# Kernel tuning notes

Hardware: AMD Instinct MI355X
Metric: run time of the kernel (lower is better)

The kernel has to match this reference:

```python
import jax, jax.numpy as jnp
import numpy as np

N = 50000          # nodes
E = 800000         # edges (before self loops)
H = 4              # attention heads
C = 64             # per-head channels
D_IN = 256
NEG_ATT = 0.2      # GATConv attention LeakyReLU slope
NEG_ACT = 0.01     # nn.LeakyReLU default slope
EPS = 1e-5
MLP_DIMS = [64, 32, 16, 2]


def _gat_layer(x, src, dst, W, a_src, a_dst, b, concat):
    """PyG GATConv: gather -> segment-softmax over dst -> scatter-add."""
    n = x.shape[0]
    h = (x @ W).reshape(n, H, C)                       # [N,H,C]
    s = (h * a_src).sum(-1)                            # [N,H]
    d = (h * a_dst).sum(-1)                            # [N,H]
    e = jax.nn.leaky_relu(s[src] + d[dst], NEG_ATT)    # [E',H]
    m = jax.ops.segment_max(e, dst, num_segments=n)    # per-dst max (self loops -> no empty segs)
    w = jnp.exp(e - m[dst])
    den = jax.ops.segment_sum(w, dst, num_segments=n)
    alpha = w / den[dst]                               # [E',H]
    out = jax.ops.segment_sum(alpha[:, :, None] * h[src], dst, num_segments=n)  # [N,H,C]
    out = out.reshape(n, H * C) if concat else out.mean(axis=1)
    return out + b


def _graph_norm(x, w, b, a):
    mu = x.mean(axis=0, keepdims=True)
    y = x - a * mu
    var = (y * y).mean(axis=0, keepdims=True)
    return w * y * jax.lax.rsqrt(var + EPS) + b


def setup_inputs() -> dict:
    key = jax.random.key(0)
    ks = jax.random.split(key, 40)
    d = {
        'x': jax.random.normal(ks[0], (N, D_IN), dtype=jnp.float32),
        'edge_index': jax.random.randint(ks[1], (2, E), 0, N, dtype=jnp.int64),
    }
    dims_in = [D_IN, H * C, H * C]
    norm_dims = [H * C, H * C, C]
    k = 2
    for i in range(3):
        fan = dims_in[i]
        d[f'W{i}'] = jax.random.normal(ks[k], (fan, H * C), dtype=jnp.float32) / np.sqrt(fan); k += 1
        d[f'as{i}'] = jax.random.normal(ks[k], (H, C), dtype=jnp.float32) / np.sqrt(C); k += 1
        d[f'ad{i}'] = jax.random.normal(ks[k], (H, C), dtype=jnp.float32) / np.sqrt(C); k += 1
        d[f'b{i}'] = jnp.zeros((norm_dims[i],), dtype=jnp.float32)
        d[f'gw{i}'] = jnp.ones((norm_dims[i],), dtype=jnp.float32)
        d[f'gb{i}'] = jnp.zeros((norm_dims[i],), dtype=jnp.float32)
        d[f'ga{i}'] = jnp.ones((norm_dims[i],), dtype=jnp.float32)
    for j in range(3):
        fi, fo = MLP_DIMS[j], MLP_DIMS[j + 1]
        d[f'mW{j}'] = jax.random.normal(ks[k], (fi, fo), dtype=jnp.float32) / np.sqrt(fi); k += 1
        d[f'mb{j}'] = jnp.zeros((fo,), dtype=jnp.float32)
    return d


def reference(x, edge_index,
              W0, as0, ad0, b0, gw0, gb0, ga0,
              W1, as1, ad1, b1, gw1, gb1, ga1,
              W2, as2, ad2, b2, gw2, gb2, ga2,
              mW0, mb0, mW1, mb1, mW2, mb2):
    n = x.shape[0]
    loop = jnp.arange(n, dtype=edge_index.dtype)
    src = jnp.concatenate([edge_index[0], loop])   # add self loops (PyG default)
    dst = jnp.concatenate([edge_index[1], loop])

    h = _gat_layer(x, src, dst, W0, as0, ad0, b0, concat=True)
    h = jax.nn.leaky_relu(_graph_norm(h, gw0, gb0, ga0), NEG_ACT)
    h = _gat_layer(h, src, dst, W1, as1, ad1, b1, concat=True)
    h = jax.nn.leaky_relu(_graph_norm(h, gw1, gb1, ga1), NEG_ACT)
    h = _gat_layer(h, src, dst, W2, as2, ad2, b2, concat=False)
    h = jax.nn.leaky_relu(_graph_norm(h, gw2, gb2, ga2), NEG_ACT)

    h = jax.nn.relu(h @ mW0 + mb0)
    h = jax.nn.relu(h @ mW1 + mb1)
    return h @ mW2 + mb2
```

## Files before the change

kernel.cpp:

```cpp
#include <hip/hip_runtime.h>

#define NN 50000
#define EE 800000
#define ET 850000
#define HH 4
#define CC 64
#define FDIM 256

#define SCAN_BLK 512
#define SCAN_NB ((NN + SCAN_BLK - 1) / SCAN_BLK)

typedef unsigned short ushort;
typedef __bf16 bf16x8 __attribute__((ext_vector_type(8)));
typedef float floatx4 __attribute__((ext_vector_type(4)));
typedef ushort ushort8v __attribute__((ext_vector_type(8)));
struct ushort4s { ushort x, y, z, w; };

__device__ __forceinline__ ushort f2bf(float f) {
  union { float f; unsigned u; } v; v.f = f;
  unsigned r = v.u + 0x7fffu + ((v.u >> 16) & 1u);
  return (ushort)(r >> 16);
}
__device__ __forceinline__ float bf2f(ushort u) {
  return __uint_as_float(((unsigned)u) << 16);
}

__device__ __forceinline__ void gload16(const void* gsrc, void* ldst) {
  __builtin_amdgcn_global_load_lds(
      (const __attribute__((address_space(1))) void*)gsrc,
      (__attribute__((address_space(3))) void*)ldst, 16, 0, 0);
}

__device__ __forceinline__ int get_edge(const void* p, int is64, long long idx) {
  if (is64) return (int)((const long long*)p)[idx];
  return ((const int*)p)[idx];
}

__global__ void degree_kernel(const void* eidx, int is64, int* deg) {
  int k = blockIdx.x * blockDim.x + threadIdx.x;
  if (k >= ET) return;
  int dst = (k < EE) ? get_edge(eidx, is64, (long long)EE + k) : (k - EE);
  atomicAdd(&deg[dst], 1);
}

__global__ __launch_bounds__(SCAN_BLK) void scan1_kernel(const int* __restrict__ deg,
                                                         int* __restrict__ rowptr,
                                                         int* __restrict__ bsum) {
  __shared__ int sm[SCAN_BLK];
  int t = threadIdx.x;
  int i = blockIdx.x * SCAN_BLK + t;
  int v = (i < NN) ? deg[i] : 0;
  sm[t] = v;
  __syncthreads();
#pragma unroll
  for (int o = 1; o < SCAN_BLK; o <<= 1) {
    int u = (t >= o) ? sm[t - o] : 0;
    __syncthreads();
    sm[t] += u;
    __syncthreads();
  }
  if (i < NN) rowptr[i] = sm[t] - v;
  if (t == SCAN_BLK - 1) bsum[blockIdx.x] = sm[t];
}

__global__ __launch_bounds__(128) void scan2_kernel(const int* __restrict__ bsum,
                                                    int* __restrict__ boff,
                                                    int* __restrict__ rowptr) {
  __shared__ int sm[128];
  int t = threadIdx.x;
  int v = (t < SCAN_NB) ? bsum[t] : 0;
  sm[t] = v;
  __syncthreads();
#pragma unroll
  for (int o = 1; o < 128; o <<= 1) {
    int u = (t >= o) ? sm[t - o] : 0;
    __syncthreads();
    sm[t] += u;
    __syncthreads();
  }
  if (t < SCAN_NB) boff[t] = sm[t] - v;
  if (t == 0) rowptr[NN] = ET;
}

__global__ __launch_bounds__(SCAN_BLK) void scan3_kernel(int* __restrict__ rowptr,
                                                         int* __restrict__ cursor,
                                                         const int* __restrict__ boff) {
  int i = blockIdx.x * SCAN_BLK + threadIdx.x;
  if (i >= NN) return;
  int v = rowptr[i] + boff[blockIdx.x];
  rowptr[i] = v;
  cursor[i] = v;
}

__global__ void fill_kernel(const void* eidx, int is64, int* cursor, int* csr_src) {
  int k = blockIdx.x * blockDim.x + threadIdx.x;
  if (k >= ET) return;
  int src, dst;
  if (k < EE) {
    src = get_edge(eidx, is64, k);
    dst = get_edge(eidx, is64, (long long)EE + k);
  } else {
    src = dst = k - EE;
  }
  int pos = atomicAdd(&cursor[dst], 1);
  csr_src[pos] = src;
}

__global__ void conv_w_kernel(const float* __restrict__ W0, const float* __restrict__ W1,
                              const float* __restrict__ W2,
                              ushort* __restrict__ T0, ushort* __restrict__ T1,
                              ushort* __restrict__ T2) {
  const float* W = (blockIdx.y == 0) ? W0 : (blockIdx.y == 1) ? W1 : W2;
  ushort* Wt = (blockIdx.y == 0) ? T0 : (blockIdx.y == 1) ? T1 : T2;
  int idx = blockIdx.x * 256 + threadIdx.x;
  int k = idx >> 8, n = idx & 255;
  Wt[n * 256 + k] = f2bf(W[idx]);
}

__global__ __launch_bounds__(256) void cvt_x_kernel(const float* __restrict__ x,
                                                    ushort* __restrict__ xb) {
  int i = blockIdx.x * 256 + threadIdx.x;
  const float4* p = (const float4*)x + (size_t)i * 2;
  float4 a = p[0], b = p[1];
  ushort8v o{f2bf(a.x), f2bf(a.y), f2bf(a.z), f2bf(a.w),
             f2bf(b.x), f2bf(b.y), f2bf(b.z), f2bf(b.w)};
  *(ushort8v*)(xb + (size_t)i * 8) = o;
}

template <int MODE>
__global__ __launch_bounds__(256) void gemm_bf16(const ushort* __restrict__ Abf,
                                                 const ushort* __restrict__ Bt,
                                                 ushort* __restrict__ C,
                                                 const float* __restrict__ as_,
                                                 const float* __restrict__ ad_,
                                                 float* __restrict__ s_arr,
                                                 float* __restrict__ d_arr,
                                                 const float* __restrict__ colsum,
                                                 const float* __restrict__ colsumsq,
                                                 const float* __restrict__ ga,
                                                 const float* __restrict__ gw,
                                                 const float* __restrict__ gb) {
  __shared__ ushort As[2][4][512];
  __shared__ ushort Bs[2][8][512];
  __shared__ float scs[FDIM], shs[FDIM];
  int tid = threadIdx.x, w = tid >> 6, l = tid & 63;
  int brow0 = blockIdx.x * 64, bcol0 = blockIdx.y * 128;
  int lm = l & 15, lk = (l >> 4) * 8;
  int arow = min(brow0 + w * 16 + lm, NN - 1);
  const ushort* ag  = Abf + (size_t)arow * 256 + lk;
  const ushort* bg0 = Bt + (size_t)(bcol0 + (2 * w) * 16 + lm) * 256 + lk;
  const ushort* bg1 = Bt + (size_t)(bcol0 + (2 * w + 1) * 16 + lm) * 256 + lk;
  ushort* lA  = &As[0][w][l * 8];
  ushort* lB0 = &Bs[0][2 * w][l * 8];
  ushort* lB1 = &Bs[0][2 * w + 1][l * 8];

  if constexpr (MODE == 1) {
    const float invn = 1.0f / (float)NN;
    float mu = colsum[tid] * invn;
    float ex2 = colsumsq[tid] * invn;
    float a = ga[tid];
    float var = fmaxf(ex2 - (2.f * a - a * a) * mu * mu, 0.f);
    float s = gw[tid] * rsqrtf(var + 1e-5f);
    scs[tid] = s;
    shs[tid] = gb[tid] - s * a * mu;
  }

  gload16(ag, lA);
  gload16(bg0, lB0);
  gload16(bg1, lB1);

  floatx4 acc[2][4];
#pragma unroll
  for (int i = 0; i < 2; i++)
#pragma unroll
    for (int j = 0; j < 4; j++) acc[i][j] = floatx4{0.f, 0.f, 0.f, 0.f};

  int wm = (w >> 1) * 2, wn = (w & 1) * 4;

#pragma unroll
  for (int s = 0; s < 8; ++s) {
    int buf = s & 1;
    __syncthreads();
    if (s < 7) {
      int k1 = (s + 1) * 32;
      int ao = (buf ^ 1) * 2048;
      int bo = (buf ^ 1) * 4096;
      gload16(ag + k1, lA + ao);
      gload16(bg0 + k1, lB0 + bo);
      gload16(bg1 + k1, lB1 + bo);
    }
    bf16x8 af[2], bfr[4];
    if constexpr (MODE == 0) {
#pragma unroll
      for (int i = 0; i < 2; i++) af[i] = *(const bf16x8*)&As[buf][wm + i][l * 8];
    } else {
      int k = s * 32 + lk;
      float4 sc0 = *(const float4*)&scs[k];
      float4 sc1 = *(const float4*)&scs[k + 4];
      float4 sh0 = *(const float4*)&shs[k];
      float4 sh1 = *(const float4*)&shs[k + 4];
#pragma unroll
      for (int i = 0; i < 2; i++) {
        ushort8v r = *(const ushort8v*)&As[buf][wm + i][l * 8];
        ushort8v a;
#pragma unroll
        for (int j = 0; j < 4; j++) {
          float y0 = fmaf(((const float*)&sc0)[j], bf2f(r[j]), ((const float*)&sh0)[j]);
          float y1 = fmaf(((const float*)&sc1)[j], bf2f(r[j + 4]), ((const float*)&sh1)[j]);
          y0 = fmaxf(y0, 0.01f * y0);
          y1 = fmaxf(y1, 0.01f * y1);
          a[j] = f2bf(y0);
          a[j + 4] = f2bf(y1);
        }
        af[i] = *(bf16x8*)&a;
      }
    }
#pragma unroll
    for (int j = 0; j < 4; j++) bfr[j] = *(const bf16x8*)&Bs[buf][wn + j][l * 8];
#pragma unroll
    for (int i = 0; i < 2; i++)
#pragma unroll
      for (int j = 0; j < 4; j++)
        acc[i][j] = __builtin_amdgcn_mfma_f32_16x16x32_bf16(af[i], bfr[j], acc[i][j], 0, 0, 0);
  }

  int quad = l >> 4;
#pragma unroll
  for (int i = 0; i < 2; i++) {
    int rr0 = brow0 + (wm + i) * 16 + quad * 4;
#pragma unroll
    for (int j = 0; j < 4; j++) {
      int col = bcol0 + (wn + j) * 16 + lm;
#pragma unroll
      for (int r = 0; r < 4; r++) {
        int row = rr0 + r;
        if (row < NN) C[(size_t)row * 256 + col] = f2bf(acc[i][j][r]);
      }
    }
  }
  float asv[4], adv[4];
#pragma unroll
  for (int j = 0; j < 4; j++) {
    int col = bcol0 + (wn + j) * 16 + lm;
    asv[j] = as_[col];
    adv[j] = ad_[col];
  }
  int head = (bcol0 >> 6) + (w & 1);
#pragma unroll
  for (int i = 0; i < 2; i++) {
#pragma unroll
    for (int r = 0; r < 4; r++) {
      float sp = acc[i][0][r] * asv[0] + acc[i][1][r] * asv[1] +
                 acc[i][2][r] * asv[2] + acc[i][3][r] * asv[3];
      float dp = acc[i][0][r] * adv[0] + acc[i][1][r] * adv[1] +
                 acc[i][2][r] * adv[2] + acc[i][3][r] * adv[3];
      sp += __shfl_xor(sp, 1); dp += __shfl_xor(dp, 1);
      sp += __shfl_xor(sp, 2); dp += __shfl_xor(dp, 2);
      sp += __shfl_xor(sp, 4); dp += __shfl_xor(dp, 4);
      sp += __shfl_xor(sp, 8); dp += __shfl_xor(dp, 8);
      if (lm == 0) {
        int row = brow0 + (wm + i) * 16 + quad * 4 + r;
        if (row < NN) {
          s_arr[row * HH + head] = sp;
          d_arr[row * HH + head] = dp;
        }
      }
    }
  }
}

template <bool CONCAT>
__global__ __launch_bounds__(256) void agg_kernel(const ushort* __restrict__ hb,
                                                  const float* __restrict__ s_arr,
                                                  const float* __restrict__ d_arr,
                                                  const int* __restrict__ rowptr,
                                                  const int* __restrict__ csr_src,
                                                  const float* __restrict__ bias,
                                                  void* __restrict__ outp) {
  int w = __builtin_amdgcn_readfirstlane(threadIdx.x >> 6);
  int l = threadIdx.x & 63;
  int head = l >> 4;
  int n = blockIdx.x * 4 + w;
  int beg = rowptr[n], end = rowptr[n + 1];
  float dh = d_arr[n * HH + head];
  float a0 = 0.f, a1 = 0.f, a2 = 0.f, a3 = 0.f, den = 0.f;

  int i = beg;
  for (; i + 16 <= end; i += 16) {
    int ss[16];
#pragma unroll
    for (int t = 0; t < 16; t++) ss[t] = csr_src[i + t];
    float ee[16];
#pragma unroll
    for (int t = 0; t < 16; t++) ee[t] = s_arr[ss[t] * HH + head];
    ushort4s hh[16];
#pragma unroll
    for (int t = 0; t < 16; t++)
      hh[t] = *(const ushort4s*)(hb + (unsigned)(ss[t] * FDIM + l * 4));
#pragma unroll
    for (int t = 0; t < 16; t++) {
      float e = ee[t] + dh;
      e = (e > 0.f) ? e : 0.2f * e;
      float wt = __expf(e);
      den += wt;
      a0 = fmaf(wt, bf2f(hh[t].x), a0);
      a1 = fmaf(wt, bf2f(hh[t].y), a1);
      a2 = fmaf(wt, bf2f(hh[t].z), a2);
      a3 = fmaf(wt, bf2f(hh[t].w), a3);
    }
  }
  for (; i + 8 <= end; i += 8) {
    int ss[8];
#pragma unroll
    for (int t = 0; t < 8; t++) ss[t] = csr_src[i + t];
    float ee[8];
#pragma unroll
    for (int t = 0; t < 8; t++) ee[t] = s_arr[ss[t] * HH + head];
    ushort4s hh[8];
#pragma unroll
    for (int t = 0; t < 8; t++)
      hh[t] = *(const ushort4s*)(hb + (unsigned)(ss[t] * FDIM + l * 4));
#pragma unroll
    for (int t = 0; t < 8; t++) {
      float e = ee[t] + dh;
      e = (e > 0.f) ? e : 0.2f * e;
      float wt = __expf(e);
      den += wt;
      a0 = fmaf(wt, bf2f(hh[t].x), a0);
      a1 = fmaf(wt, bf2f(hh[t].y), a1);
      a2 = fmaf(wt, bf2f(hh[t].z), a2);
      a3 = fmaf(wt, bf2f(hh[t].w), a3);
    }
  }
  for (; i + 4 <= end; i += 4) {
    int ss[4];
#pragma unroll
    for (int t = 0; t < 4; t++) ss[t] = csr_src[i + t];
    float ee[4];
#pragma unroll
    for (int t = 0; t < 4; t++) ee[t] = s_arr[ss[t] * HH + head];
    ushort4s hh[4];
#pragma unroll
    for (int t = 0; t < 4; t++)
      hh[t] = *(const ushort4s*)(hb + (unsigned)(ss[t] * FDIM + l * 4));
#pragma unroll
    for (int t = 0; t < 4; t++) {
      float e = ee[t] + dh;
      e = (e > 0.f) ? e : 0.2f * e;
      float wt = __expf(e);
      den += wt;
      a0 = fmaf(wt, bf2f(hh[t].x), a0);
      a1 = fmaf(wt, bf2f(hh[t].y), a1);
      a2 = fmaf(wt, bf2f(hh[t].z), a2);
      a3 = fmaf(wt, bf2f(hh[t].w), a3);
    }
  }
  for (; i < end; i++) {
    int s0 = csr_src[i];
    float e0 = s_arr[s0 * HH + head] + dh;
    ushort4s h0 = *(const ushort4s*)(hb + (unsigned)(s0 * FDIM + l * 4));
    e0 = (e0 > 0.f) ? e0 : 0.2f * e0;
    float w0 = __expf(e0);
    den += w0;
    a0 = fmaf(w0, bf2f(h0.x), a0); a1 = fmaf(w0, bf2f(h0.y), a1);
    a2 = fmaf(w0, bf2f(h0.z), a2); a3 = fmaf(w0, bf2f(h0.w), a3);
  }
  float inv = 1.0f / den;
  float r0 = a0 * inv, r1 = a1 * inv, r2 = a2 * inv, r3 = a3 * inv;

  if (CONCAT) {
    float4 bv = ((const float4*)bias)[l];
    ushort4s o;
    o.x = f2bf(r0 + bv.x); o.y = f2bf(r1 + bv.y);
    o.z = f2bf(r2 + bv.z); o.w = f2bf(r3 + bv.w);
    ((ushort4s*)outp)[(unsigned)(n * 64 + l)] = o;
  } else {
    r0 += __shfl_xor(r0, 16); r1 += __shfl_xor(r1, 16);
    r2 += __shfl_xor(r2, 16); r3 += __shfl_xor(r3, 16);
    r0 += __shfl_xor(r0, 32); r1 += __shfl_xor(r1, 32);
    r2 += __shfl_xor(r2, 32); r3 += __shfl_xor(r3, 32);
    if (l < 16) {
      float4 bv = ((const float4*)bias)[l];
      float4 o;
      o.x = 0.25f * r0 + bv.x; o.y = 0.25f * r1 + bv.y;
      o.z = 0.25f * r2 + bv.z; o.w = 0.25f * r3 + bv.w;
      ((float4*)outp)[(unsigned)(n * 16 + l)] = o;
    }
  }
}

__global__ __launch_bounds__(256) void norm_reduce_bf(const ushort* __restrict__ xin,
                                                      float* colsum, float* colsumsq) {
  __shared__ float4 sm1[256], sm2[256];
  int t = threadIdx.x;
  int c4 = (t & 63) * 4;
  int rl = t >> 6;
  int r0 = blockIdx.x * 128;
  int r1 = min(NN, r0 + 128);
  float s0 = 0.f, s1 = 0.f, s2 = 0.f, s3 = 0.f;
  float q0 = 0.f, q1 = 0.f, q2 = 0.f, q3 = 0.f;
  for (int r = r0 + rl; r < r1; r += 4) {
    ushort4s v = *(const ushort4s*)(xin + (size_t)r * FDIM + c4);
    float f0 = bf2f(v.x), f1 = bf2f(v.y), f2 = bf2f(v.z), f3 = bf2f(v.w);
    s0 += f0; q0 += f0 * f0;
    s1 += f1; q1 += f1 * f1;
    s2 += f2; q2 += f2 * f2;
    s3 += f3; q3 += f3 * f3;
  }
  sm1[t] = float4{s0, s1, s2, s3};
  sm2[t] = float4{q0, q1, q2, q3};
  __syncthreads();
  if (t < 64) {
    float4 a = sm1[t], b = sm1[t + 64], c = sm1[t + 128], d = sm1[t + 192];
    atomicAdd(&colsum[c4 + 0], a.x + b.x + c.x + d.x);
    atomicAdd(&colsum[c4 + 1], a.y + b.y + c.y + d.y);
    atomicAdd(&colsum[c4 + 2], a.z + b.z + c.z + d.z);
    atomicAdd(&colsum[c4 + 3], a.w + b.w + c.w + d.w);
    float4 e = sm2[t], f = sm2[t + 64], g = sm2[t + 128], h = sm2[t + 192];
    atomicAdd(&colsumsq[c4 + 0], e.x + f.x + g.x + h.x);
    atomicAdd(&colsumsq[c4 + 1], e.y + f.y + g.y + h.y);
    atomicAdd(&colsumsq[c4 + 2], e.z + f.z + g.z + h.z);
    atomicAdd(&colsumsq[c4 + 3], e.w + f.w + g.w + h.w);
  }
}

__global__ __launch_bounds__(256) void norm_reduce_f32(const float* __restrict__ xin,
                                                       float* colsum, float* colsumsq) {
  int f = threadIdx.x & (CC - 1);
  int rl = threadIdx.x / CC;
  int r0 = blockIdx.x * 128;
  int r1 = min(NN, r0 + 128);
  float s1 = 0.f, s2 = 0.f;
  for (int r = r0 + rl; r < r1; r += 4) {
    float v = xin[(size_t)r * CC + f];
    s1 += v; s2 += v * v;
  }
  atomicAdd(&colsum[f], s1);
  atomicAdd(&colsumsq[f], s2);
}

__global__ __launch_bounds__(256) void mlp_kernel(const float* __restrict__ xin,
                                                  const float* __restrict__ colsum,
                                                  const float* __restrict__ colsumsq,
                                                  const float* __restrict__ ga,
                                                  const float* __restrict__ gw,
                                                  const float* __restrict__ gb,
                                                  const float* mW0, const float* mb0,
                                                  const float* mW1, const float* mb1,
                                                  const float* mW2, const float* mb2,
                                                  float* __restrict__ out) {
  __shared__ float W0s[64 * 32];
  __shared__ float W1s[32 * 16];
  __shared__ float W2s[16 * 2];
  __shared__ float b0s[32], b1s[16], b2s[2];
  __shared__ float sc[CC], sh[CC];
  int t = threadIdx.x;
  for (int i = t; i < 2048; i += 256) W0s[i] = mW0[i];
  for (int i = t; i < 512; i += 256) W1s[i] = mW1[i];
  if (t < 32) { W2s[t] = mW2[t]; b0s[t] = mb0[t]; }
  if (t < 16) b1s[t] = mb1[t];
  if (t < 2) b2s[t] = mb2[t];
  if (t < CC) {
    const float invn = 1.0f / (float)NN;
    float mu = colsum[t] * invn;
    float ex2 = colsumsq[t] * invn;
    float a = ga[t];
    float var = fmaxf(ex2 - (2.f * a - a * a) * mu * mu, 0.f);
    float s = gw[t] * rsqrtf(var + 1e-5f);
    sc[t] = s; sh[t] = gb[t] - s * a * mu;
  }
  __syncthreads();
  int node = blockIdx.x * 256 + t;
  if (node >= NN) return;
  float in[64];
  const float* xr = xin + (size_t)node * 64;
#pragma unroll
  for (int k = 0; k < 64; k++) {
    float y = sc[k] * xr[k] + sh[k];
    in[k] = (y > 0.f) ? y : 0.01f * y;
  }
  float h1[32];
#pragma unroll
  for (int j = 0; j < 32; j++) h1[j] = b0s[j];
#pragma unroll
  for (int k = 0; k < 64; k++) {
    float v = in[k];
#pragma unroll
    for (int j = 0; j < 32; j++) h1[j] += v * W0s[k * 32 + j];
  }
#pragma unroll
  for (int j = 0; j < 32; j++) h1[j] = fmaxf(h1[j], 0.f);
  float h2[16];
#pragma unroll
  for (int j = 0; j < 16; j++) h2[j] = b1s[j];
#pragma unroll
  for (int k = 0; k < 32; k++) {
    float v = h1[k];
#pragma unroll
    for (int j = 0; j < 16; j++) h2[j] += v * W1s[k * 16 + j];
  }
#pragma unroll
  for (int j = 0; j < 16; j++) h2[j] = fmaxf(h2[j], 0.f);
  float o0 = b2s[0], o1 = b2s[1];
#pragma unroll
  for (int k = 0; k < 16; k++) {
    o0 += h2[k] * W2s[k * 2 + 0];
    o1 += h2[k] * W2s[k * 2 + 1];
  }
  out[(size_t)node * 2 + 0] = o0;
  out[(size_t)node * 2 + 1] = o1;
}

extern "C" void kernel_launch(void* const* d_in, const int* in_sizes, int n_in,
                              void* d_out, int out_size, void* d_ws, size_t ws_size,
                              hipStream_t stream) {
  const float* x = (const float*)d_in[0];
  const void* ei = d_in[1];
  const float* W[3]   = {(const float*)d_in[2],  (const float*)d_in[9],  (const float*)d_in[16]};
  const float* as_[3] = {(const float*)d_in[3],  (const float*)d_in[10], (const float*)d_in[17]};
  const float* ad_[3] = {(const float*)d_in[4],  (const float*)d_in[11], (const float*)d_in[18]};
  const float* b_[3]  = {(const float*)d_in[5],  (const float*)d_in[12], (const float*)d_in[19]};
  const float* gw[3]  = {(const float*)d_in[6],  (const float*)d_in[13], (const float*)d_in[20]};
  const float* gb[3]  = {(const float*)d_in[7],  (const float*)d_in[14], (const float*)d_in[21]};
  const float* ga[3]  = {(const float*)d_in[8],  (const float*)d_in[15], (const float*)d_in[22]};
  const float* mW0 = (const float*)d_in[23];
  const float* mb0 = (const float*)d_in[24];
  const float* mW1 = (const float*)d_in[25];
  const float* mb1 = (const float*)d_in[26];
  const float* mW2 = (const float*)d_in[27];
  const float* mb2 = (const float*)d_in[28];
  float* out = (float*)d_out;

  int is64 = (in_sizes[1] == (int)(2u * EE * 8u)) ? 1 : 0;

  char* ws = (char*)d_ws;
  size_t off = 0;
  auto take = [&](size_t bytes) -> char* {
    char* p = ws + off;
    off = (off + bytes + 255) & ~(size_t)255;
    return p;
  };
  ushort* hb    = (ushort*)take((size_t)NN * FDIM * 2);
  ushort* aggb  = (ushort*)take((size_t)NN * FDIM * 2);
  ushort* xbf   = (ushort*)take((size_t)NN * FDIM * 2);
  float* bufD   = (float*)take((size_t)NN * CC * 4);
  ushort* Wt[3];
  for (int i = 0; i < 3; i++) Wt[i] = (ushort*)take((size_t)256 * 256 * 2);
  float* s_arr  = (float*)take((size_t)NN * HH * 4);
  float* d_arr  = (float*)take((size_t)NN * HH * 4);
  char* zbase   = (char*)take(0);
  int* deg      = (int*)take((size_t)NN * 4);
  float* cs[3];
  for (int i = 0; i < 3; i++) cs[i] = (float*)take(2048);
  size_t zlen   = (size_t)(((char*)cs[2] + 2048) - zbase);
  int* cursor   = (int*)take((size_t)NN * 4);
  int* rowptr   = (int*)take((size_t)(NN + 1) * 4);
  int* csr_src  = (int*)take((size_t)ET * 4);
  int* bsum     = (int*)take(512);
  int* boff     = (int*)take(512);

  hipMemsetAsync(zbase, 0, zlen, stream);

  degree_kernel<<<(ET + 255) / 256, 256, 0, stream>>>(ei, is64, deg);
  scan1_kernel<<<SCAN_NB, SCAN_BLK, 0, stream>>>(deg, rowptr, bsum);
  scan2_kernel<<<1, 128, 0, stream>>>(bsum, boff, rowptr);
  scan3_kernel<<<SCAN_NB, SCAN_BLK, 0, stream>>>(rowptr, cursor, boff);
  fill_kernel<<<(ET + 255) / 256, 256, 0, stream>>>(ei, is64, cursor, csr_src);

  conv_w_kernel<<<dim3(256, 3), 256, 0, stream>>>(W[0], W[1], W[2], Wt[0], Wt[1], Wt[2]);
  cvt_x_kernel<<<(NN * FDIM / 8 + 255) / 256, 256, 0, stream>>>(x, xbf);

  dim3 ggrid((NN + 63) / 64, 2);
  for (int L = 0; L < 3; L++) {
    if (L == 0)
      gemm_bf16<0><<<ggrid, 256, 0, stream>>>(xbf, Wt[0], hb,
                                              as_[0], ad_[0], s_arr, d_arr,
                                              nullptr, nullptr, nullptr, nullptr, nullptr);
    else
      gemm_bf16<1><<<ggrid, 256, 0, stream>>>(aggb, Wt[L], hb,
                                              as_[L], ad_[L], s_arr, d_arr,
                                              cs[L - 1], cs[L - 1] + 256,
                                              ga[L - 1], gw[L - 1], gb[L - 1]);
    if (L < 2) {
      agg_kernel<true><<<NN / 4, 256, 0, stream>>>(hb, s_arr, d_arr, rowptr, csr_src, b_[L], aggb);
      norm_reduce_bf<<<(NN + 127) / 128, 256, 0, stream>>>(aggb, cs[L], cs[L] + 256);
    } else {
      agg_kernel<false><<<NN / 4, 256, 0, stream>>>(hb, s_arr, d_arr, rowptr, csr_src, b_[L], bufD);
      norm_reduce_f32<<<(NN + 127) / 128, 256, 0, stream>>>(bufD, cs[2], cs[2] + 256);
    }
  }
  mlp_kernel<<<(NN + 255) / 256, 256, 0, stream>>>(bufD, cs[2], cs[2] + 256,
                                                   ga[2], gw[2], gb[2],
                                                   mW0, mb0, mW1, mb1, mW2, mb2, out);
}
```

Before: 692.3 us.

## Unfuse graph-norm from GEMM prologue and double K-step per pipeline stage

Removes the fused graph-norm plus LeakyReLU transform from the GEMM A-fragment load and puts it in a separate elementwise norm_apply kernel, which writes normalized bf16 activations back into the x buffer. The GEMM becomes a single non-templated version that stages 64 K-columns per step (4 iterations instead of 8) with doubled LDS buffers. The aim is to take per-fragment ALU work out of the MFMA loop and halve the number of barriers. In exchange it adds an extra full read and write of the 50000x256 bf16 activation buffer and two more kernel launches.

```diff
diff --git a/kernel.cpp b/kernel.cpp
--- a/kernel.cpp
+++ b/kernel.cpp
@@ -127,22 +127,49 @@
   *(ushort8v*)(xb + (size_t)i * 8) = o;
 }
 
-template <int MODE>
+__global__ __launch_bounds__(256) void norm_apply_kernel(const ushort* __restrict__ xin,
+                                                         ushort* __restrict__ xout,
+                                                         const float* __restrict__ colsum,
+                                                         const float* __restrict__ colsumsq,
+                                                         const float* __restrict__ ga,
+                                                         const float* __restrict__ gw,
+                                                         const float* __restrict__ gb) {
+  __shared__ float scs[FDIM], shs[FDIM];
+  int t = threadIdx.x;
+  {
+    const float invn = 1.0f / (float)NN;
+    float mu = colsum[t] * invn;
+    float ex2 = colsumsq[t] * invn;
+    float a = ga[t];
+    float var = fmaxf(ex2 - (2.f * a - a * a) * mu * mu, 0.f);
+    float s = gw[t] * rsqrtf(var + 1e-5f);
+    scs[t] = s;
+    shs[t] = gb[t] - s * a * mu;
+  }
+  __syncthreads();
+  int idx = blockIdx.x * 256 + t;
+  int c0 = (idx & 31) * 8;
+  size_t off = (size_t)(idx >> 5) * 256 + c0;
+  ushort8v r = *(const ushort8v*)(xin + off);
+  ushort8v o;
+#pragma unroll
+  for (int j = 0; j < 8; j++) {
+    float y = fmaf(scs[c0 + j], bf2f(r[j]), shs[c0 + j]);
+    y = fmaxf(y, 0.01f * y);
+    o[j] = f2bf(y);
+  }
+  *(ushort8v*)(xout + off) = o;
+}
+
 __global__ __launch_bounds__(256) void gemm_bf16(const ushort* __restrict__ Abf,
                                                  const ushort* __restrict__ Bt,
                                                  ushort* __restrict__ C,
                                                  const float* __restrict__ as_,
                                                  const float* __restrict__ ad_,
                                                  float* __restrict__ s_arr,
-                                                 float* __restrict__ d_arr,
-                                                 const float* __restrict__ colsum,
-                                                 const float* __restrict__ colsumsq,
-                                                 const float* __restrict__ ga,
-                                                 const float* __restrict__ gw,
-                                                 const float* __restrict__ gb) {
-  __shared__ ushort As[2][4][512];
-  __shared__ ushort Bs[2][8][512];
-  __shared__ float scs[FDIM], shs[FDIM];
+                                                 float* __restrict__ d_arr) {
+  __shared__ ushort As[2][2][4][512];
+  __shared__ ushort Bs[2][2][8][512];
   int tid = threadIdx.x, w = tid >> 6, l = tid & 63;
   int brow0 = blockIdx.x * 64, bcol0 = blockIdx.y * 128;
   int lm = l & 15, lk = (l >> 4) * 8;
@@ -150,24 +177,18 @@
   const ushort* ag  = Abf + (size_t)arow * 256 + lk;
   const ushort* bg0 = Bt + (size_t)(bcol0 + (2 * w) * 16 + lm) * 256 + lk;
   const ushort* bg1 = Bt + (size_t)(bcol0 + (2 * w + 1) * 16 + lm) * 256 + lk;
-  ushort* lA  = &As[0][w][l * 8];
-  ushort* lB0 = &Bs[0][2 * w][l * 8];
-  ushort* lB1 = &Bs[0][2 * w + 1][l * 8];
-
-  if constexpr (MODE == 1) {
-    const float invn = 1.0f / (float)NN;
-    float mu = colsum[tid] * invn;
-    float ex2 = colsumsq[tid] * invn;
-    float a = ga[tid];
-    float var = fmaxf(ex2 - (2.f * a - a * a) * mu * mu, 0.f);
-    float s = gw[tid] * rsqrtf(var + 1e-5f);
-    scs[tid] = s;
-    shs[tid] = gb[tid] - s * a * mu;
-  }
-
-  gload16(ag, lA);
-  gload16(bg0, lB0);
-  gload16(bg1, lB1);
+
+  auto stage = [&](int buf, int s) {
+#pragma unroll
+    for (int c = 0; c < 2; c++) {
+      int go = s * 64 + c * 32;
+      gload16(ag + go, &As[buf][c][w][l * 8]);
+      gload16(bg0 + go, &Bs[buf][c][2 * w][l * 8]);
+      gload16(bg1 + go, &Bs[buf][c][2 * w + 1][l * 8]);
+    }
+  };
+
+  stage(0, 0);
 
   floatx4 acc[2][4];
 #pragma unroll
@@ -178,50 +199,23 @@
   int wm = (w >> 1) * 2, wn = (w & 1) * 4;
 
 #pragma unroll
-  for (int s = 0; s < 8; ++s) {
+  for (int s = 0; s < 4; ++s) {
     int buf = s & 1;
     __syncthreads();
-    if (s < 7) {
-      int k1 = (s + 1) * 32;
-      int ao = (buf ^ 1) * 2048;
-      int bo = (buf ^ 1) * 4096;
-      gload16(ag + k1, lA + ao);
-      gload16(bg0 + k1, lB0 + bo);
-      gload16(bg1 + k1, lB1 + bo);
-    }
-    bf16x8 af[2], bfr[4];
-    if constexpr (MODE == 0) {
-#pragma unroll
-      for (int i = 0; i < 2; i++) af[i] = *(const bf16x8*)&As[buf][wm + i][l * 8];
-    } else {
-      int k = s * 32 + lk;
-      float4 sc0 = *(const float4*)&scs[k];
-      float4 sc1 = *(const float4*)&scs[k + 4];
-      float4 sh0 = *(const float4*)&shs[k];
-      float4 sh1 = *(const float4*)&shs[k + 4];
-#pragma unroll
-      for (int i = 0; i < 2; i++) {
-        ushort8v r = *(const ushort8v*)&As[buf][wm + i][l * 8];
-        ushort8v a;
-#pragma unroll
-        for (int j = 0; j < 4; j++) {
-          float y0 = fmaf(((const float*)&sc0)[j], bf2f(r[j]), ((const float*)&sh0)[j]);
-          float y1 = fmaf(((const float*)&sc1)[j], bf2f(r[j + 4]), ((const float*)&sh1)[j]);
-          y0 = fmaxf(y0, 0.01f * y0);
-          y1 = fmaxf(y1, 0.01f * y1);
-          a[j] = f2bf(y0);
-          a[j + 4] = f2bf(y1);
-        }
-        af[i] = *(bf16x8*)&a;
-      }
-    }
-#pragma unroll
-    for (int j = 0; j < 4; j++) bfr[j] = *(const bf16x8*)&Bs[buf][wn + j][l * 8];
-#pragma unroll
-    for (int i = 0; i < 2; i++)
-#pragma unroll
-      for (int j = 0; j < 4; j++)
-        acc[i][j] = __builtin_amdgcn_mfma_f32_16x16x32_bf16(af[i], bfr[j], acc[i][j], 0, 0, 0);
+    if (s < 3) stage(buf ^ 1, s + 1);
+#pragma unroll
+    for (int c = 0; c < 2; c++) {
+      bf16x8 af[2], bfr[4];
+#pragma unroll
+      for (int i = 0; i < 2; i++) af[i] = *(const bf16x8*)&As[buf][c][wm + i][l * 8];
+#pragma unroll
+      for (int j = 0; j < 4; j++) bfr[j] = *(const bf16x8*)&Bs[buf][c][wn + j][l * 8];
+#pragma unroll
+      for (int i = 0; i < 2; i++)
+#pragma unroll
+        for (int j = 0; j < 4; j++)
+          acc[i][j] = __builtin_amdgcn_mfma_f32_16x16x32_bf16(af[i], bfr[j], acc[i][j], 0, 0, 0);
+    }
   }
 
   int quad = l >> 4;
@@ -571,19 +565,14 @@
   cvt_x_kernel<<<(NN * FDIM / 8 + 255) / 256, 256, 0, stream>>>(x, xbf);
 
   dim3 ggrid((NN + 63) / 64, 2);
+  int napply = NN * FDIM / 8 / 256;
   for (int L = 0; L < 3; L++) {
-    if (L == 0)
-      gemm_bf16<0><<<ggrid, 256, 0, stream>>>(xbf, Wt[0], hb,
-                                              as_[0], ad_[0], s_arr, d_arr,
-                                              nullptr, nullptr, nullptr, nullptr, nullptr);
-    else
-      gemm_bf16<1><<<ggrid, 256, 0, stream>>>(aggb, Wt[L], hb,
-                                              as_[L], ad_[L], s_arr, d_arr,
-                                              cs[L - 1], cs[L - 1] + 256,
-                                              ga[L - 1], gw[L - 1], gb[L - 1]);
+    gemm_bf16<<<ggrid, 256, 0, stream>>>(xbf, Wt[L], hb, as_[L], ad_[L], s_arr, d_arr);
     if (L < 2) {
       agg_kernel<true><<<NN / 4, 256, 0, stream>>>(hb, s_arr, d_arr, rowptr, csr_src, b_[L], aggb);
       norm_reduce_bf<<<(NN + 127) / 128, 256, 0, stream>>>(aggb, cs[L], cs[L] + 256);
+      norm_apply_kernel<<<napply, 256, 0, stream>>>(aggb, xbf, cs[L], cs[L] + 256,
+                                                    ga[L], gw[L], gb[L]);
     } else {
       agg_kernel<false><<<NN / 4, 256, 0, stream>>>(hb, s_arr, d_arr, rowptr, csr_src, b_[L], bufD);
       norm_reduce_f32<<<(NN + 127) / 128, 256, 0, stream>>>(bufD, cs[2], cs[2] + 256);
```

New measurement: 710.4 us. +2.6%, slower.
